# Kernel tuning notes

Measured on AMD Instinct MI355X. Metric: run time of the kernel, lower is better.

Reference implementation:

```python
import jax, jax.numpy as jnp
import numpy as np

N = 50000      # B*N nodes
K = 32         # top-k in-degree
E = N * K      # edges
IN_DIM = 128
EMB_DIM = 128
OUT_DIM = 128
HEADS = 4
D_HEAD = OUT_DIM // HEADS


def setup_inputs() -> dict:
    key = jax.random.key(0)
    ks = jax.random.split(key, 8)
    x = jax.random.normal(ks[0], (N, IN_DIM), dtype=jnp.float32)
    emb = jax.random.normal(ks[1], (N, EMB_DIM), dtype=jnp.float32)
    # top-k graph: each node i has exactly K in-neighbors (dst covers all nodes)
    dst = jnp.repeat(jnp.arange(N, dtype=jnp.int32), K)
    src = jax.random.randint(ks[2], (E,), 0, N, dtype=jnp.int32)
    edge_index = jnp.stack([src, dst], axis=0)
    # learned params (stored as (in, out); math-equivalent to torch Linear)
    W_q = jax.random.normal(ks[3], (EMB_DIM, OUT_DIM), dtype=jnp.float32) / np.sqrt(EMB_DIM)
    W_k = jax.random.normal(ks[4], (EMB_DIM, OUT_DIM), dtype=jnp.float32) / np.sqrt(EMB_DIM)
    W_v = jax.random.normal(ks[5], (IN_DIM + EMB_DIM, OUT_DIM), dtype=jnp.float32) / np.sqrt(IN_DIM + EMB_DIM)
    attn_vec = jax.random.normal(ks[6], (HEADS, 2 * D_HEAD), dtype=jnp.float32) / np.sqrt(2 * D_HEAD)
    ln_gamma = jnp.ones((OUT_DIM,), dtype=jnp.float32)
    ln_beta = jnp.zeros((OUT_DIM,), dtype=jnp.float32)
    return {"x": x, "emb": emb, "edge_index": edge_index, "W_q": W_q, "W_k": W_k,
            "W_v": W_v, "attn_vec": attn_vec, "ln_gamma": ln_gamma, "ln_beta": ln_beta}


def reference(x, emb, edge_index, W_q, W_k, W_v, attn_vec, ln_gamma, ln_beta):
    src, dst = edge_index[0], edge_index[1]
    BN = x.shape[0]
    H, D = HEADS, D_HEAD
    Q = (emb @ W_q).reshape(BN, H, D)
    K_ = (emb @ W_k).reshape(BN, H, D)
    # a^T [q_dst || k_src] = (a_q . q)_dst + (a_k . k)_src  (standard GAT split)
    a_q, a_k = attn_vec[:, :D], attn_vec[:, D:]
    sq = jnp.einsum('nhd,hd->nh', Q, a_q)   # (BN, H)
    sk = jnp.einsum('nhd,hd->nh', K_, a_k)  # (BN, H)
    e = sq[dst] + sk[src]                   # (E, H)
    e = jnp.where(e > 0, e, 0.2 * e)        # LeakyReLU(0.2)
    # segment softmax over incoming edges of each dst node
    e_max = jax.ops.segment_max(e, dst, num_segments=BN)
    e_exp = jnp.exp(e - e_max[dst])
    e_sum = jax.ops.segment_sum(e_exp, dst, num_segments=BN)
    alpha = e_exp / (e_sum[dst] + 1e-8)     # (E, H); dropout is identity at eval
    V = (jnp.concatenate([x, emb], axis=-1) @ W_v).reshape(BN, H, D)
    weighted = alpha[..., None] * V[src]    # (E, H, D)
    z = jax.ops.segment_sum(weighted, dst, num_segments=BN).reshape(BN, H * D)
    z = jax.nn.elu(z)
    mu = jnp.mean(z, axis=-1, keepdims=True)
    var = jnp.var(z, axis=-1, keepdims=True)
    return (z - mu) / jnp.sqrt(var + 1e-5) * ln_gamma + ln_beta
```

## Files before the change

### kernel.cpp

```cpp
#include <hip/hip_runtime.h>

#define NN 50000
#define KE 32

using f32x4  = __attribute__((ext_vector_type(4))) float;
using bf16x8 = __attribute__((ext_vector_type(8))) short;

__device__ __forceinline__ ushort f2bf(float f) {
    union { float f; unsigned u; } c; c.f = f;
    unsigned u = c.u;
    u += 0x7fffu + ((u >> 16) & 1u);
    return (ushort)(u >> 16);
}

__global__ __launch_bounds__(256) void prep_kernel(const float* __restrict__ Wq,
        const float* __restrict__ Wk, const float* __restrict__ av,
        const float* __restrict__ Wv, float* __restrict__ u, float* __restrict__ v,
        ushort* __restrict__ Bt) {
    const int g = blockIdx.x * 256 + threadIdx.x;
    if (blockIdx.x < 2) {
        const int h = g >> 7, i = g & 127;
        float su = 0.f, sv = 0.f;
#pragma unroll
        for (int d = 0; d < 32; ++d) {
            su += Wq[i * 128 + h * 32 + d] * av[h * 64 + d];
            sv += Wk[i * 128 + h * 32 + d] * av[h * 64 + 32 + d];
        }
        u[h * 128 + i] = su;
        v[h * 128 + i] = sv;
    } else {
        const int idx = g - 512;
        const int k = idx >> 7, n = idx & 127;
        Bt[n * 256 + k] = f2bf(Wv[idx]);
    }
}

__global__ __launch_bounds__(256) void vproj_mfma(const float* __restrict__ x,
        const float* __restrict__ emb, const ushort* __restrict__ Bt,
        ushort* __restrict__ Vb) {
    __shared__ short As[64 * 264];
    const int t = threadIdx.x;
    const int rbase = blockIdx.x * 64;

#pragma unroll
    for (int it = 0; it < 16; ++it) {
        const int li = it * 256 + t;
        const int row = li >> 6;
        const int c4 = li & 63;
        int rg = rbase + row; if (rg >= NN) rg = NN - 1;
        const float* sp = (c4 < 32) ? (x + (long)rg * 128 + c4 * 4)
                                    : (emb + (long)rg * 128 + (c4 - 32) * 4);
        float4 a = *(const float4*)sp;
        ushort4 b = make_ushort4(f2bf(a.x), f2bf(a.y), f2bf(a.z), f2bf(a.w));
        *(ushort4*)&As[row * 264 + c4 * 4] = b;
    }
    __syncthreads();

    const int wv = t >> 6;
    const int lane = t & 63;
    const int lo = lane & 15;
    const int quad = lane >> 4;
    const int c0 = wv * 32;

    f32x4 acc[4][2] = {};
    for (int ks = 0; ks < 8; ++ks) {
        const int kb = ks * 32 + quad * 8;
        bf16x8 bf0 = *(const bf16x8*)(Bt + (c0 + lo) * 256 + kb);
        bf16x8 bf1 = *(const bf16x8*)(Bt + (c0 + 16 + lo) * 256 + kb);
#pragma unroll
        for (int rt = 0; rt < 4; ++rt) {
            bf16x8 af = *(const bf16x8*)&As[(rt * 16 + lo) * 264 + kb];
            acc[rt][0] = __builtin_amdgcn_mfma_f32_16x16x32_bf16(af, bf0, acc[rt][0], 0, 0, 0);
            acc[rt][1] = __builtin_amdgcn_mfma_f32_16x16x32_bf16(af, bf1, acc[rt][1], 0, 0, 0);
        }
    }
#pragma unroll
    for (int rt = 0; rt < 4; ++rt) {
#pragma unroll
        for (int ct = 0; ct < 2; ++ct) {
#pragma unroll
            for (int r = 0; r < 4; ++r) {
                const int row = rbase + rt * 16 + quad * 4 + r;
                if (row < NN)
                    Vb[(long)row * 128 + c0 + ct * 16 + lo] = f2bf(acc[rt][ct][r]);
            }
        }
    }
}

__global__ __launch_bounds__(256) void score_kernel(const float* __restrict__ emb,
        const float* __restrict__ u, const float* __restrict__ v,
        float* __restrict__ sq, float* __restrict__ sk) {
    const int w = threadIdx.x >> 6;
    const int lane = threadIdx.x & 63;
    const int n = blockIdx.x * 4 + w;
    const float ea = emb[(long)n * 128 + lane];
    const float eb = emb[(long)n * 128 + 64 + lane];
    float q[4], k_[4];
#pragma unroll
    for (int h = 0; h < 4; ++h) {
        float pu = ea * u[h * 128 + lane] + eb * u[h * 128 + 64 + lane];
        float pv = ea * v[h * 128 + lane] + eb * v[h * 128 + 64 + lane];
#pragma unroll
        for (int off = 32; off > 0; off >>= 1) {
            pu += __shfl_xor(pu, off);
            pv += __shfl_xor(pv, off);
        }
        q[h] = pu; k_[h] = pv;
    }
    if (lane == 0) {
        *(float4*)(sq + (long)n * 4) = make_float4(q[0], q[1], q[2], q[3]);
        *(float4*)(sk + (long)n * 4) = make_float4(k_[0], k_[1], k_[2], k_[3]);
    }
}

__global__ __launch_bounds__(256) void aggregate_kernel(const int* __restrict__ src,
        const float* __restrict__ sq, const float* __restrict__ sk,
        const ushort* __restrict__ Vb, const float* __restrict__ gamma,
        const float* __restrict__ beta, float* __restrict__ out) {
    __shared__ int s_src[4][32];
    __shared__ float4 s_alpha[4][32];
    const int w = threadIdx.x >> 6;
    const int lane = threadIdx.x & 63;
    const int n = blockIdx.x * 4 + w;

    if (lane < 32) {
        const int s = src[(long)n * KE + lane];
        float4 sk4 = *(const float4*)(sk + (long)s * 4);
        float4 sq4 = *(const float4*)(sq + (long)n * 4);
        float e[4] = { sq4.x + sk4.x, sq4.y + sk4.y, sq4.z + sk4.z, sq4.w + sk4.w };
#pragma unroll
        for (int h = 0; h < 4; ++h) e[h] = e[h] > 0.f ? e[h] : 0.2f * e[h];
        float m[4] = { e[0], e[1], e[2], e[3] };
#pragma unroll
        for (int off = 16; off > 0; off >>= 1) {
#pragma unroll
            for (int h = 0; h < 4; ++h) m[h] = fmaxf(m[h], __shfl_xor(m[h], off));
        }
        float ex[4], sum[4];
#pragma unroll
        for (int h = 0; h < 4; ++h) { ex[h] = __expf(e[h] - m[h]); sum[h] = ex[h]; }
#pragma unroll
        for (int off = 16; off > 0; off >>= 1) {
#pragma unroll
            for (int h = 0; h < 4; ++h) sum[h] += __shfl_xor(sum[h], off);
        }
        float4 al;
        al.x = ex[0] / (sum[0] + 1e-8f);
        al.y = ex[1] / (sum[1] + 1e-8f);
        al.z = ex[2] / (sum[2] + 1e-8f);
        al.w = ex[3] / (sum[3] + 1e-8f);
        s_src[w][lane] = s;
        s_alpha[w][lane] = al;
    }
    __syncthreads();

    const int c0 = lane * 2;
    const int h = lane >> 4;
    float zx = 0.f, zy = 0.f;
#pragma unroll 8
    for (int e = 0; e < 32; ++e) {
        const int s = s_src[w][e];
        const float a = ((const float*)&s_alpha[w][e])[h];
        const unsigned p = *(const unsigned*)(Vb + (long)s * 128 + c0);
        union { unsigned u; float f; } vx, vy;
        vx.u = p << 16;
        vy.u = p & 0xffff0000u;
        zx += a * vx.f;
        zy += a * vy.f;
    }
    zx = zx > 0.f ? zx : __expf(zx) - 1.f;
    zy = zy > 0.f ? zy : __expf(zy) - 1.f;
    float s1 = zx + zy;
    float s2 = zx * zx + zy * zy;
#pragma unroll
    for (int off = 32; off > 0; off >>= 1) {
        s1 += __shfl_xor(s1, off);
        s2 += __shfl_xor(s2, off);
    }
    const float mu = s1 * (1.f / 128.f);
    const float var = s2 * (1.f / 128.f) - mu * mu;
    const float rstd = rsqrtf(var + 1e-5f);
    float2 g = *(const float2*)(gamma + c0);
    float2 b = *(const float2*)(beta + c0);
    float2 o;
    o.x = (zx - mu) * rstd * g.x + b.x;
    o.y = (zy - mu) * rstd * g.y + b.y;
    *(float2*)(out + (long)n * 128 + c0) = o;
}

extern "C" void kernel_launch(void* const* d_in, const int* in_sizes, int n_in,
                              void* d_out, int out_size, void* d_ws, size_t ws_size,
                              hipStream_t stream) {
    const float* x     = (const float*)d_in[0];
    const float* emb   = (const float*)d_in[1];
    const int*   edge  = (const int*)d_in[2];
    const float* Wq    = (const float*)d_in[3];
    const float* Wk    = (const float*)d_in[4];
    const float* Wv    = (const float*)d_in[5];
    const float* av    = (const float*)d_in[6];
    const float* gamma = (const float*)d_in[7];
    const float* beta  = (const float*)d_in[8];
    float* out = (float*)d_out;

    char* ws = (char*)d_ws;
    float*  u  = (float*)(ws + 0);
    float*  v  = (float*)(ws + 2048);
    float*  sq = (float*)(ws + 4096);
    float*  sk = (float*)(ws + 804096);
    ushort* Bt = (ushort*)(ws + 1604096);
    ushort* Vb = (ushort*)(ws + 1669632);

    prep_kernel<<<130, 256, 0, stream>>>(Wq, Wk, av, Wv, u, v, Bt);
    vproj_mfma<<<(NN + 63) / 64, 256, 0, stream>>>(x, emb, Bt, Vb);
    score_kernel<<<NN / 4, 256, 0, stream>>>(emb, u, v, sq, sk);
    aggregate_kernel<<<NN / 4, 256, 0, stream>>>(edge, sq, sk, Vb, gamma, beta, out);
}
```

Baseline: 197.0 us.

## Fuse attention score projection into V-projection MFMA kernel and widen aggregate gathers

Removes the separate score kernel by computing sq/sk inside the V-projection kernel with an extra bf16 MFMA against packed projection vectors, reusing the emb tile already staged in shared memory. The V output is staged through LDS so it can be written with 16-byte coalesced stores. The aggregate kernel now gathers 16-byte V rows, with four lane groups each handling a subset of edges and combining results through shuffles. This saves one launch and one full read of emb, and cuts the number of gather transactions, at the cost of bf16 precision on the scores and extra shuffles.

```diff
diff --git a/kernel.cpp b/kernel.cpp
--- a/kernel.cpp
+++ b/kernel.cpp
@@ -15,7 +15,7 @@
 
 __global__ __launch_bounds__(256) void prep_kernel(const float* __restrict__ Wq,
         const float* __restrict__ Wk, const float* __restrict__ av,
-        const float* __restrict__ Wv, float* __restrict__ u, float* __restrict__ v,
+        const float* __restrict__ Wv, ushort* __restrict__ Ub,
         ushort* __restrict__ Bt) {
     const int g = blockIdx.x * 256 + threadIdx.x;
     if (blockIdx.x < 2) {
@@ -26,8 +26,10 @@
             su += Wq[i * 128 + h * 32 + d] * av[h * 64 + d];
             sv += Wk[i * 128 + h * 32 + d] * av[h * 64 + 32 + d];
         }
-        u[h * 128 + i] = su;
-        v[h * 128 + i] = sv;
+        Ub[h * 128 + i] = f2bf(su);
+        Ub[(4 + h) * 128 + i] = f2bf(sv);
+        Ub[1024 + g * 2] = 0;
+        Ub[1024 + g * 2 + 1] = 0;
     } else {
         const int idx = g - 512;
         const int k = idx >> 7, n = idx & 127;
@@ -37,7 +39,8 @@
 
 __global__ __launch_bounds__(256) void vproj_mfma(const float* __restrict__ x,
         const float* __restrict__ emb, const ushort* __restrict__ Bt,
-        ushort* __restrict__ Vb) {
+        const ushort* __restrict__ Ub, float* __restrict__ sq,
+        float* __restrict__ sk, ushort* __restrict__ Vb) {
     __shared__ short As[64 * 264];
     const int t = threadIdx.x;
     const int rbase = blockIdx.x * 64;
@@ -74,43 +77,45 @@
             acc[rt][1] = __builtin_amdgcn_mfma_f32_16x16x32_bf16(af, bf1, acc[rt][1], 0, 0, 0);
         }
     }
-#pragma unroll
-    for (int rt = 0; rt < 4; ++rt) {
-#pragma unroll
-        for (int ct = 0; ct < 2; ++ct) {
-#pragma unroll
-            for (int r = 0; r < 4; ++r) {
-                const int row = rbase + rt * 16 + quad * 4 + r;
-                if (row < NN)
-                    Vb[(long)row * 128 + c0 + ct * 16 + lo] = f2bf(acc[rt][ct][r]);
+
+    f32x4 sacc = {};
+#pragma unroll
+    for (int ks = 0; ks < 4; ++ks) {
+        const int kk = ks * 32 + quad * 8;
+        bf16x8 saf = *(const bf16x8*)&As[(wv * 16 + lo) * 264 + 128 + kk];
+        bf16x8 sbf = *(const bf16x8*)(Ub + lo * 128 + kk);
+        sacc = __builtin_amdgcn_mfma_f32_16x16x32_bf16(saf, sbf, sacc, 0, 0, 0);
+    }
+    if (lo < 8) {
+#pragma unroll
+        for (int r = 0; r < 4; ++r) {
+            const int row = rbase + wv * 16 + quad * 4 + r;
+            if (row < NN) {
+                if (lo < 4) sq[(long)row * 4 + lo] = sacc[r];
+                else        sk[(long)row * 4 + lo - 4] = sacc[r];
             }
         }
     }
-}
-
-__global__ __launch_bounds__(256) void score_kernel(const float* __restrict__ emb,
-        const float* __restrict__ u, const float* __restrict__ v,
-        float* __restrict__ sq, float* __restrict__ sk) {
-    const int w = threadIdx.x >> 6;
-    const int lane = threadIdx.x & 63;
-    const int n = blockIdx.x * 4 + w;
-    const float ea = emb[(long)n * 128 + lane];
-    const float eb = emb[(long)n * 128 + 64 + lane];
-    float q[4], k_[4];
-#pragma unroll
-    for (int h = 0; h < 4; ++h) {
-        float pu = ea * u[h * 128 + lane] + eb * u[h * 128 + 64 + lane];
-        float pv = ea * v[h * 128 + lane] + eb * v[h * 128 + 64 + lane];
-#pragma unroll
-        for (int off = 32; off > 0; off >>= 1) {
-            pu += __shfl_xor(pu, off);
-            pv += __shfl_xor(pv, off);
-        }
-        q[h] = pu; k_[h] = pv;
-    }
-    if (lane == 0) {
-        *(float4*)(sq + (long)n * 4) = make_float4(q[0], q[1], q[2], q[3]);
-        *(float4*)(sk + (long)n * 4) = make_float4(k_[0], k_[1], k_[2], k_[3]);
+
+    __syncthreads();
+#pragma unroll
+    for (int rt = 0; rt < 4; ++rt)
+#pragma unroll
+        for (int ct = 0; ct < 2; ++ct)
+#pragma unroll
+            for (int r = 0; r < 4; ++r)
+                As[(rt * 16 + quad * 4 + r) * 132 + c0 + ct * 16 + lo] =
+                    (short)f2bf(acc[rt][ct][r]);
+    __syncthreads();
+#pragma unroll
+    for (int i = 0; i < 4; ++i) {
+        const int idx = i * 256 + t;
+        const int row = idx >> 4;
+        const int seg = idx & 15;
+        const int grow = rbase + row;
+        if (grow < NN)
+            *(bf16x8*)(Vb + (long)grow * 128 + seg * 8) =
+                *(const bf16x8*)&As[row * 132 + seg * 8];
     }
 }
 
@@ -155,38 +160,57 @@
     }
     __syncthreads();
 
-    const int c0 = lane * 2;
-    const int h = lane >> 4;
-    float zx = 0.f, zy = 0.f;
-#pragma unroll 8
-    for (int e = 0; e < 32; ++e) {
+    const int g  = lane >> 4;
+    const int li = lane & 15;
+    const int h  = li >> 2;
+    float z[8] = {};
+#pragma unroll
+    for (int it = 0; it < 8; ++it) {
+        const int e = it * 4 + g;
         const int s = s_src[w][e];
         const float a = ((const float*)&s_alpha[w][e])[h];
-        const unsigned p = *(const unsigned*)(Vb + (long)s * 128 + c0);
-        union { unsigned u; float f; } vx, vy;
-        vx.u = p << 16;
-        vy.u = p & 0xffff0000u;
-        zx += a * vx.f;
-        zy += a * vy.f;
-    }
-    zx = zx > 0.f ? zx : __expf(zx) - 1.f;
-    zy = zy > 0.f ? zy : __expf(zy) - 1.f;
-    float s1 = zx + zy;
-    float s2 = zx * zx + zy * zy;
-#pragma unroll
-    for (int off = 32; off > 0; off >>= 1) {
+        uint4 p = *(const uint4*)(Vb + (long)s * 128 + li * 8);
+        const unsigned pc[4] = { p.x, p.y, p.z, p.w };
+#pragma unroll
+        for (int j = 0; j < 4; ++j) {
+            union { unsigned u; float f; } ve, vo;
+            ve.u = pc[j] << 16;
+            vo.u = pc[j] & 0xffff0000u;
+            z[2 * j]     += a * ve.f;
+            z[2 * j + 1] += a * vo.f;
+        }
+    }
+#pragma unroll
+    for (int j = 0; j < 8; ++j) {
+        z[j] += __shfl_xor(z[j], 16);
+        z[j] += __shfl_xor(z[j], 32);
+    }
+    float s1 = 0.f, s2 = 0.f;
+#pragma unroll
+    for (int j = 0; j < 8; ++j) {
+        z[j] = z[j] > 0.f ? z[j] : __expf(z[j]) - 1.f;
+        s1 += z[j];
+        s2 += z[j] * z[j];
+    }
+#pragma unroll
+    for (int off = 8; off > 0; off >>= 1) {
         s1 += __shfl_xor(s1, off);
         s2 += __shfl_xor(s2, off);
     }
     const float mu = s1 * (1.f / 128.f);
     const float var = s2 * (1.f / 128.f) - mu * mu;
     const float rstd = rsqrtf(var + 1e-5f);
-    float2 g = *(const float2*)(gamma + c0);
-    float2 b = *(const float2*)(beta + c0);
-    float2 o;
-    o.x = (zx - mu) * rstd * g.x + b.x;
-    o.y = (zy - mu) * rstd * g.y + b.y;
-    *(float2*)(out + (long)n * 128 + c0) = o;
+    if (g < 2) {
+        const int c0 = li * 8 + g * 4;
+        float4 ga = *(const float4*)(gamma + c0);
+        float4 be = *(const float4*)(beta + c0);
+        float4 o;
+        o.x = (z[g * 4 + 0] - mu) * rstd * ga.x + be.x;
+        o.y = (z[g * 4 + 1] - mu) * rstd * ga.y + be.y;
+        o.z = (z[g * 4 + 2] - mu) * rstd * ga.z + be.z;
+        o.w = (z[g * 4 + 3] - mu) * rstd * ga.w + be.w;
+        *(float4*)(out + (long)n * 128 + c0) = o;
+    }
 }
 
 extern "C" void kernel_launch(void* const* d_in, const int* in_sizes, int n_in,
@@ -204,15 +228,13 @@
     float* out = (float*)d_out;
 
     char* ws = (char*)d_ws;
-    float*  u  = (float*)(ws + 0);
-    float*  v  = (float*)(ws + 2048);
-    float*  sq = (float*)(ws + 4096);
-    float*  sk = (float*)(ws + 804096);
-    ushort* Bt = (ushort*)(ws + 1604096);
+    ushort* Ub = (ushort*)(ws + 0);
+    ushort* Bt = (ushort*)(ws + 4096);
+    float*  sq = (float*)(ws + 69632);
+    float*  sk = (float*)(ws + 869632);
     ushort* Vb = (ushort*)(ws + 1669632);
 
-    prep_kernel<<<130, 256, 0, stream>>>(Wq, Wk, av, Wv, u, v, Bt);
-    vproj_mfma<<<(NN + 63) / 64, 256, 0, stream>>>(x, emb, Bt, Vb);
-    score_kernel<<<NN / 4, 256, 0, stream>>>(emb, u, v, sq, sk);
+    prep_kernel<<<130, 256, 0, stream>>>(Wq, Wk, av, Wv, Ub, Bt);
+    vproj_mfma<<<(NN + 63) / 64, 256, 0, stream>>>(x, emb, Bt, Ub, sq, sk, Vb);
     aggregate_kernel<<<NN / 4, 256, 0, stream>>>(edge, sq, sk, Vb, gamma, beta, out);
 }
```

Result: faster. 178.2 us (-9.5%).
